# Performance work log

Hardware: AMD Instinct MI355X
Metric: run time of the kernel (lower is better)

The kernel has to match this reference:

```python
import jax, jax.numpy as jnp
import numpy as np

# Flax nn.LSTMCell math: gates order (i, f, g, o); input Dense has no bias,
# hidden Dense has bias (merged here into a single bias b per direction).
# new_c = sigmoid(f)*c + sigmoid(i)*tanh(g); new_h = sigmoid(o)*tanh(new_c)

def _run_lstm(xs, Wx, Wh, b):
    # xs: [S, B, E]; Wx: [E, 4H]; Wh: [H, 4H]; b: [4H]
    B = xs.shape[1]
    H = Wh.shape[0]
    def step(carry, x):
        h, c = carry
        gates = x @ Wx + h @ Wh + b            # [B, 4H]
        i, f, g, o = jnp.split(gates, 4, axis=-1)
        c = jax.nn.sigmoid(f) * c + jax.nn.sigmoid(i) * jnp.tanh(g)
        h = jax.nn.sigmoid(o) * jnp.tanh(c)
        return (h, c), h
    init = (jnp.zeros((B, H), xs.dtype), jnp.zeros((B, H), xs.dtype))
    (h, c), hs = jax.lax.scan(step, init, xs)
    return hs, h, c


def setup_inputs() -> dict:
    key = jax.random.key(0)
    ks = jax.random.split(key, 8)
    V, E, H = 32000, 1024, 1024
    B, S = 64, 512
    inputs = jax.random.randint(ks[0], (B, S), 0, V, dtype=jnp.int32)
    embed_table = jax.random.normal(ks[1], (V, E), dtype=jnp.float32) * 0.02
    Wx_f = jax.random.normal(ks[2], (E, 4 * H), dtype=jnp.float32) * 0.02
    Wh_f = jax.random.normal(ks[3], (H, 4 * H), dtype=jnp.float32) * 0.02
    b_f = jnp.zeros((4 * H,), dtype=jnp.float32)
    Wx_b = jax.random.normal(ks[4], (E, 4 * H), dtype=jnp.float32) * 0.02
    Wh_b = jax.random.normal(ks[5], (H, 4 * H), dtype=jnp.float32) * 0.02
    b_b = jnp.zeros((4 * H,), dtype=jnp.float32)
    return {"inputs": inputs, "embed_table": embed_table,
            "Wx_f": Wx_f, "Wh_f": Wh_f, "b_f": b_f,
            "Wx_b": Wx_b, "Wh_b": Wh_b, "b_b": b_b}


def reference(inputs, embed_table, Wx_f, Wh_f, b_f, Wx_b, Wh_b, b_b):
    emb = embed_table[inputs]                  # [B, S, E]
    xs = jnp.transpose(emb, (1, 0, 2))         # [S, B, E] for scan
    # Forward direction
    hs_f, h_f, c_f = _run_lstm(xs, Wx_f, Wh_f, b_f)
    # Backward direction: reverse time, run, reverse outputs back
    hs_b, h_b, c_b = _run_lstm(xs[::-1], Wx_b, Wh_b, b_b)
    hs_b = hs_b[::-1]
    outputs = jnp.concatenate([hs_f, hs_b], axis=-1)   # [S, B, 2H]
    outputs = jnp.transpose(outputs, (1, 0, 2))        # [B, S, 2H]
    hidden = jnp.concatenate([h_f, h_b], axis=-1)      # [B, 2H]
    cell = jnp.concatenate([c_f, c_b], axis=-1)        # [B, 2H]
    return outputs, hidden, cell
```

## Files before the change

### kernel.cpp

```cpp
#include <hip/hip_runtime.h>
#include <stdint.h>

typedef __attribute__((ext_vector_type(8))) short short8;
typedef __attribute__((ext_vector_type(4))) float floatx4;

#define S_LEN 512
#define BATCH 64
#define HID   1024
#define GATES 4096
#define EMB   1024
#define M_ROWS 32768

__device__ __forceinline__ short f2bf(float f) {
  unsigned u = __float_as_uint(f);
  unsigned r = (u + 0x7fffu + ((u >> 16) & 1u)) >> 16;
  return (short)r;
}
__device__ __forceinline__ float bf2f(short v) {
  return __uint_as_float(((unsigned)(unsigned short)v) << 16);
}
__device__ __forceinline__ void ld_lds16(const void* g, void* l) {
  __builtin_amdgcn_global_load_lds((const __attribute__((address_space(1))) void*)g,
                                   (__attribute__((address_space(3))) void*)l, 16, 0, 0);
}

__global__ __launch_bounds__(256) void k_gather(const int* __restrict__ tok,
                                                const float* __restrict__ table,
                                                short* __restrict__ X) {
  int r = blockIdx.x;
  int b = r & 63, s = r >> 6;
  int t = tok[b * S_LEN + s];
  const float* src = table + (size_t)t * EMB;
  short* dst = X + (size_t)r * EMB;
  for (int k = threadIdx.x; k < EMB; k += 256) dst[k] = f2bf(src[k]);
}

__global__ __launch_bounds__(256) void k_transpose(const float* __restrict__ W,
                                                   short* __restrict__ WT) {
  __shared__ short tile[32][33];
  int k0 = blockIdx.x * 32, n0 = blockIdx.y * 32;
  int tx = threadIdx.x & 31, ty = threadIdx.x >> 5;
#pragma unroll
  for (int i = 0; i < 32; i += 8)
    tile[ty + i][tx] = f2bf(W[(size_t)(k0 + ty + i) * GATES + n0 + tx]);
  __syncthreads();
#pragma unroll
  for (int i = 0; i < 32; i += 8)
    WT[(size_t)(n0 + ty + i) * HID + k0 + tx] = tile[tx][ty + i];
}

__global__ __launch_bounds__(256) void k_zero(uint32_t* p, int n) {
  int i = blockIdx.x * 256 + threadIdx.x;
  if (i < n) p[i] = 0u;
}

__global__ __launch_bounds__(256) void k_gemm_in(const short* __restrict__ X,
                                                 const short* __restrict__ WT_f,
                                                 const short* __restrict__ WT_b,
                                                 const float* __restrict__ bias_f,
                                                 const float* __restrict__ bias_b,
                                                 short* __restrict__ Gin_f,
                                                 short* __restrict__ Gin_b) {
  const short* WT   = blockIdx.z ? WT_b : WT_f;
  const float* bias = blockIdx.z ? bias_b : bias_f;
  short* Gin        = blockIdx.z ? Gin_b : Gin_f;
  __shared__ __align__(16) short sA[128 * 32];
  __shared__ __align__(16) short sB[128 * 32];
  int tid = threadIdx.x;
  int lane = tid & 63, wave = tid >> 6;
  int n0 = blockIdx.x * 128, m0 = blockIdx.y * 128;
  int wm = (wave & 1) * 64, wn = (wave >> 1) * 64;
  int lm = lane & 15, lk = (lane >> 4) * 8;
  floatx4 acc[4][4];
  for (int i = 0; i < 4; i++)
    for (int j = 0; j < 4; j++)
      for (int r = 0; r < 4; r++) acc[i][j][r] = 0.f;

  for (int kt = 0; kt < HID; kt += 32) {
    __syncthreads();
#pragma unroll
    for (int i = 0; i < 2; i++) {
      int c = tid + i * 256;
      int row = c >> 2, k8 = (c & 3) * 8;
      ld_lds16(X + (size_t)(m0 + row) * HID + kt + k8, sA + c * 8);
    }
#pragma unroll
    for (int i = 0; i < 2; i++) {
      int c = tid + i * 256;
      int row = c >> 2, k8 = (c & 3) * 8;
      ld_lds16(WT + (size_t)(n0 + row) * HID + kt + k8, sB + c * 8);
    }
    __syncthreads();
    short8 af[4], bf4[4];
#pragma unroll
    for (int mi = 0; mi < 4; mi++) af[mi] = *(const short8*)&sA[(wm + mi * 16 + lm) * 32 + lk];
#pragma unroll
    for (int ni = 0; ni < 4; ni++) bf4[ni] = *(const short8*)&sB[(wn + ni * 16 + lm) * 32 + lk];
#pragma unroll
    for (int mi = 0; mi < 4; mi++)
#pragma unroll
      for (int ni = 0; ni < 4; ni++)
        acc[mi][ni] = __builtin_amdgcn_mfma_f32_16x16x32_bf16(af[mi], bf4[ni], acc[mi][ni], 0, 0, 0);
  }
  int lr = lane >> 4;
#pragma unroll
  for (int mi = 0; mi < 4; mi++)
    for (int ni = 0; ni < 4; ni++)
      for (int r = 0; r < 4; r++) {
        int m = m0 + wm + mi * 16 + lr * 4 + r;
        int n = n0 + wn + ni * 16 + lm;
        Gin[(size_t)m * GATES + n] = f2bf(acc[mi][ni][r] + bias[n]);
      }
}

__global__ __launch_bounds__(256) void k_step(
    int t, int fused,
    const short* __restrict__ Gin_f, const short* __restrict__ Gin_b,
    const short* __restrict__ X,
    const short* __restrict__ WxT_f, const short* __restrict__ WxT_b,
    const float* __restrict__ bias_f, const float* __restrict__ bias_b,
    const short* __restrict__ WhT_f, const short* __restrict__ WhT_b,
    const short* __restrict__ hin_f, const short* __restrict__ hin_b,
    short* __restrict__ hout_f, short* __restrict__ hout_b,
    float* __restrict__ c_f, float* __restrict__ c_b,
    float* __restrict__ out) {
  int wg = blockIdx.x;
  int dir = wg >> 6;
  int j0 = (wg & 63) * 16;
  int tid = threadIdx.x, lane = tid & 63, g = tid >> 6;
  int lm = lane & 15, lk = (lane >> 4) * 8, lr = lane >> 4;
  int s = dir ? (S_LEN - 1 - t) : t;
  const short* WhT = dir ? WhT_b : WhT_f;
  const short* hin = dir ? hin_b : hin_f;
  short* hout = dir ? hout_b : hout_f;
  float* cbuf = dir ? c_b : c_f;
  int ncol = g * HID + j0 + lm;

  floatx4 acc[4];
  for (int mt = 0; mt < 4; mt++)
    for (int r = 0; r < 4; r++) acc[mt][r] = 0.f;

  {
    const short* Wrow = WhT + (size_t)ncol * HID;
#pragma unroll 4
    for (int kt = 0; kt < HID; kt += 32) {
      short8 bfrag = *(const short8*)&Wrow[kt + lk];
#pragma unroll
      for (int mt = 0; mt < 4; mt++) {
        short8 afrag = *(const short8*)&hin[(mt * 16 + lm) * HID + kt + lk];
        acc[mt] = __builtin_amdgcn_mfma_f32_16x16x32_bf16(afrag, bfrag, acc[mt], 0, 0, 0);
      }
    }
  }
  if (fused) {
    const short* Wrow = (dir ? WxT_b : WxT_f) + (size_t)ncol * HID;
    const short* Xb = X + (size_t)s * BATCH * EMB;
#pragma unroll 4
    for (int kt = 0; kt < EMB; kt += 32) {
      short8 bfrag = *(const short8*)&Wrow[kt + lk];
#pragma unroll
      for (int mt = 0; mt < 4; mt++) {
        short8 afrag = *(const short8*)&Xb[(mt * 16 + lm) * EMB + kt + lk];
        acc[mt] = __builtin_amdgcn_mfma_f32_16x16x32_bf16(afrag, bfrag, acc[mt], 0, 0, 0);
      }
    }
  }

  __shared__ float gl[4][64][16];
  const short* Gin = dir ? Gin_b : Gin_f;
  const float* bias = dir ? bias_b : bias_f;
#pragma unroll
  for (int mt = 0; mt < 4; mt++)
    for (int r = 0; r < 4; r++) {
      int m = mt * 16 + lr * 4 + r;
      float v = acc[mt][r];
      if (fused) v += bias[ncol];
      else       v += bf2f(Gin[(size_t)(s * BATCH + m) * GATES + ncol]);
      gl[g][m][lm] = v;
    }
  __syncthreads();

  for (int p = tid; p < BATCH * 16; p += 256) {
    int m = p >> 4, nl = p & 15;
    int hcol = j0 + nl;
    float iv = gl[0][m][nl], fv = gl[1][m][nl], gv = gl[2][m][nl], ov = gl[3][m][nl];
    float co = cbuf[m * HID + hcol];
    float si = 1.f / (1.f + __expf(-iv));
    float sf = 1.f / (1.f + __expf(-fv));
    float so = 1.f / (1.f + __expf(-ov));
    float cn = sf * co + si * tanhf(gv);
    float hn = so * tanhf(cn);
    cbuf[m * HID + hcol] = cn;
    hout[m * HID + hcol] = f2bf(hn);
    out[(size_t)m * (S_LEN * 2 * HID) + (size_t)s * (2 * HID) + dir * HID + hcol] = hn;
    if (t == S_LEN - 1) {
      size_t hid_base = (size_t)BATCH * S_LEN * 2 * HID;
      out[hid_base + (size_t)m * (2 * HID) + dir * HID + hcol] = hn;
      out[hid_base + (size_t)BATCH * 2 * HID + (size_t)m * (2 * HID) + dir * HID + hcol] = cn;
    }
  }
}

extern "C" void kernel_launch(void* const* d_in, const int* in_sizes, int n_in,
                              void* d_out, int out_size, void* d_ws, size_t ws_size,
                              hipStream_t stream) {
  const int*   tok   = (const int*)d_in[0];
  const float* table = (const float*)d_in[1];
  const float* Wx_f  = (const float*)d_in[2];
  const float* Wh_f  = (const float*)d_in[3];
  const float* b_f   = (const float*)d_in[4];
  const float* Wx_b  = (const float*)d_in[5];
  const float* Wh_b  = (const float*)d_in[6];
  const float* b_b   = (const float*)d_in[7];
  float* out = (float*)d_out;

  char* w = (char*)d_ws;
  short* WxTf = (short*)(w + 0);
  short* WxTb = (short*)(w + 8388608);
  short* WhTf = (short*)(w + 16777216);
  short* WhTb = (short*)(w + 25165824);
  char* state = w + 33554432;
  short* h_f1 = (short*)(state);
  short* h_b1 = (short*)(state + 131072);
  float* c_f  = (float*)(state + 262144);
  float* c_b  = (float*)(state + 524288);
  short* h_f2 = (short*)(state + 786432);
  short* h_b2 = (short*)(state + 917504);
  short* X    = (short*)(w + 34603008);
  short* Ginf = (short*)(w + 101711872);
  short* Ginb = (short*)(w + 370147328);
  int fused = (ws_size < 638582784ull) ? 1 : 0;

  k_gather<<<dim3(M_ROWS), dim3(256), 0, stream>>>(tok, table, X);
  k_transpose<<<dim3(32, 128), dim3(256), 0, stream>>>(Wx_f, WxTf);
  k_transpose<<<dim3(32, 128), dim3(256), 0, stream>>>(Wx_b, WxTb);
  k_transpose<<<dim3(32, 128), dim3(256), 0, stream>>>(Wh_f, WhTf);
  k_transpose<<<dim3(32, 128), dim3(256), 0, stream>>>(Wh_b, WhTb);
  k_zero<<<dim3(768), dim3(256), 0, stream>>>((uint32_t*)state, 786432 / 4);
  if (!fused)
    k_gemm_in<<<dim3(32, 256, 2), dim3(256), 0, stream>>>(X, WxTf, WxTb, b_f, b_b, Ginf, Ginb);

  for (int t = 0; t < S_LEN; t++) {
    const short* hinf = (t & 1) ? h_f2 : h_f1;
    const short* hinb = (t & 1) ? h_b2 : h_b1;
    short* houtf = (t & 1) ? h_f1 : h_f2;
    short* houtb = (t & 1) ? h_b1 : h_b2;
    k_step<<<dim3(128), dim3(256), 0, stream>>>(t, fused, Ginf, Ginb, X, WxTf, WxTb, b_f, b_b,
                                                WhTf, WhTb, hinf, hinb, houtf, houtb, c_f, c_b, out);
  }
}
```

Measured before the change: 16.23 ms.

## Replace per-timestep launches with persistent cooperative recurrence kernel holding Wh in registers

Adds a persistent cooperative kernel that runs all 512 timesteps of both LSTM directions in one launch, using grid.sync between steps instead of 512 separate kernel launches. Each workgroup keeps its slice of the recurrent weight matrix in registers across all steps and keeps the cell state in registers too. This is meant to remove per-step launch overhead and the repeated reloading of Wh from memory. The cost is a grid-wide barrier per step, heavy register pressure (64 short8 arrays per lane), and a fallback to the old launch loop if the cooperative launch fails.

```diff
diff --git a/kernel.cpp b/kernel.cpp
--- a/kernel.cpp
+++ b/kernel.cpp
@@ -1,4 +1,5 @@
 #include <hip/hip_runtime.h>
+#include <hip/hip_cooperative_groups.h>
 #include <stdint.h>
 
 typedef __attribute__((ext_vector_type(8))) short short8;
@@ -201,6 +202,103 @@
   }
 }
 
+__global__ __launch_bounds__(256, 1) void k_recur(
+    const short* __restrict__ Gin_f, const short* __restrict__ Gin_b,
+    const short* __restrict__ WhT_f, const short* __restrict__ WhT_b,
+    short* __restrict__ hf1, short* __restrict__ hf2,
+    short* __restrict__ hb1, short* __restrict__ hb2,
+    float* __restrict__ out) {
+  cooperative_groups::grid_group grid = cooperative_groups::this_grid();
+  int wg = blockIdx.x;
+  int dir = wg >> 7;
+  int j0 = (wg & 127) * 8;
+  int tid = threadIdx.x;
+  int w = tid >> 6;
+  int lane = tid & 63;
+  int lm = lane & 15, lr = lane >> 4;
+  int lk = lr * 8;
+  const short* WhT = dir ? WhT_b : WhT_f;
+  const short* Gin = dir ? Gin_b : Gin_f;
+  short* hin  = dir ? hb1 : hf1;
+  short* hout = dir ? hb2 : hf2;
+
+  int gc0 = ((lm >> 3) << 10) + j0 + (lm & 7);
+  int gc1 = gc0 + 2048;
+  int rowbase = w * 16 + lr * 4;
+
+  short8 wr0[32], wr1[32];
+#pragma unroll
+  for (int kt = 0; kt < 32; kt++) {
+    wr0[kt] = *(const short8*)&WhT[(size_t)gc0 * HID + kt * 32 + lk];
+    wr1[kt] = *(const short8*)&WhT[(size_t)gc1 * HID + kt * 32 + lk];
+  }
+
+  float c0 = 0.f, c1 = 0.f;
+  int rbase = (lm < 8) ? 0 : 2;
+  int hcol = j0 + (lm & 7);
+
+  for (int t = 0; t < S_LEN; t++) {
+    int s = dir ? (S_LEN - 1 - t) : t;
+
+    const short* gin = Gin + (size_t)s * BATCH * GATES;
+    short gv0[4], gv1[4];
+#pragma unroll
+    for (int r = 0; r < 4; r++) {
+      gv0[r] = gin[(size_t)(rowbase + r) * GATES + gc0];
+      gv1[r] = gin[(size_t)(rowbase + r) * GATES + gc1];
+    }
+
+    floatx4 acc0 = {0.f, 0.f, 0.f, 0.f};
+    floatx4 acc1 = {0.f, 0.f, 0.f, 0.f};
+    const short* hrow = hin + (size_t)(w * 16 + lm) * HID;
+#pragma unroll
+    for (int kt = 0; kt < 32; kt++) {
+      short8 a = *(const short8*)&hrow[kt * 32 + lk];
+      acc0 = __builtin_amdgcn_mfma_f32_16x16x32_bf16(a, wr0[kt], acc0, 0, 0, 0);
+      acc1 = __builtin_amdgcn_mfma_f32_16x16x32_bf16(a, wr1[kt], acc1, 0, 0, 0);
+    }
+#pragma unroll
+    for (int r = 0; r < 4; r++) {
+      acc0[r] += bf2f(gv0[r]);
+      acc1[r] += bf2f(gv1[r]);
+    }
+
+    float sw0[4], sw1[4];
+#pragma unroll
+    for (int r = 0; r < 4; r++) {
+      sw0[r] = __shfl_xor(acc0[r], 8, 64);
+      sw1[r] = __shfl_xor(acc1[r], 8, 64);
+    }
+
+#pragma unroll
+    for (int rr = 0; rr < 2; rr++) {
+      int r = rbase + rr;
+      float iv = (lm < 8) ? acc0[r] : sw0[r];
+      float fv = (lm < 8) ? sw0[r] : acc0[r];
+      float gg = (lm < 8) ? acc1[r] : sw1[r];
+      float ov = (lm < 8) ? sw1[r] : acc1[r];
+      float cprev = rr ? c1 : c0;
+      float si = 1.f / (1.f + __expf(-iv));
+      float sf = 1.f / (1.f + __expf(-fv));
+      float so = 1.f / (1.f + __expf(-ov));
+      float cn = sf * cprev + si * tanhf(gg);
+      float hn = so * tanhf(cn);
+      if (rr) c1 = cn; else c0 = cn;
+      int row = rowbase + r;
+      hout[row * HID + hcol] = f2bf(hn);
+      out[(size_t)row * (S_LEN * 2 * HID) + (size_t)s * (2 * HID) + dir * HID + hcol] = hn;
+      if (t == S_LEN - 1) {
+        size_t hid_base = (size_t)BATCH * S_LEN * 2 * HID;
+        out[hid_base + (size_t)row * (2 * HID) + dir * HID + hcol] = hn;
+        out[hid_base + (size_t)BATCH * 2 * HID + (size_t)row * (2 * HID) + dir * HID + hcol] = cn;
+      }
+    }
+
+    grid.sync();
+    short* tmp = hin; hin = hout; hout = tmp;
+  }
+}
+
 extern "C" void kernel_launch(void* const* d_in, const int* in_sizes, int n_in,
                               void* d_out, int out_size, void* d_ws, size_t ws_size,
                               hipStream_t stream) {
@@ -237,15 +335,30 @@
   k_transpose<<<dim3(32, 128), dim3(256), 0, stream>>>(Wh_f, WhTf);
   k_transpose<<<dim3(32, 128), dim3(256), 0, stream>>>(Wh_b, WhTb);
   k_zero<<<dim3(768), dim3(256), 0, stream>>>((uint32_t*)state, 786432 / 4);
-  if (!fused)
+
+  int use_persistent = 0;
+  if (!fused) {
     k_gemm_in<<<dim3(32, 256, 2), dim3(256), 0, stream>>>(X, WxTf, WxTb, b_f, b_b, Ginf, Ginb);
-
-  for (int t = 0; t < S_LEN; t++) {
-    const short* hinf = (t & 1) ? h_f2 : h_f1;
-    const short* hinb = (t & 1) ? h_b2 : h_b1;
-    short* houtf = (t & 1) ? h_f1 : h_f2;
-    short* houtb = (t & 1) ? h_b1 : h_b2;
-    k_step<<<dim3(128), dim3(256), 0, stream>>>(t, fused, Ginf, Ginb, X, WxTf, WxTb, b_f, b_b,
-                                                WhTf, WhTb, hinf, hinb, houtf, houtb, c_f, c_b, out);
-  }
-}
+    void* args[9];
+    args[0] = (void*)&Ginf;  args[1] = (void*)&Ginb;
+    args[2] = (void*)&WhTf;  args[3] = (void*)&WhTb;
+    args[4] = (void*)&h_f1;  args[5] = (void*)&h_f2;
+    args[6] = (void*)&h_b1;  args[7] = (void*)&h_b2;
+    args[8] = (void*)&out;
+    hipError_t err = hipLaunchCooperativeKernel((const void*)k_recur, dim3(256), dim3(256),
+                                                args, 0, stream);
+    if (err == hipSuccess) use_persistent = 1;
+    else (void)hipGetLastError();
+  }
+
+  if (!use_persistent) {
+    for (int t = 0; t < S_LEN; t++) {
+      const short* hinf = (t & 1) ? h_f2 : h_f1;
+      const short* hinb = (t & 1) ? h_b2 : h_b1;
+      short* houtf = (t & 1) ? h_f1 : h_f2;
+      short* houtb = (t & 1) ? h_b1 : h_b2;
+      k_step<<<dim3(128), dim3(256), 0, stream>>>(t, fused, Ginf, Ginb, X, WxTf, WxTb, b_f, b_b,
+                                                  WhTf, WhTb, hinf, hinb, houtf, houtb, c_f, c_b, out);
+    }
+  }
+}
```

Measured after the change: 20.72 ms. 27.7% more time.
